# Kernel tuning notes

Hardware: AMD Instinct MI355X
Metric: run time of the kernel (lower is better)

The kernel has to match this reference:

```python
import jax, jax.numpy as jnp
import numpy as np

B, S, E, H = 8, 2048, 1024, 64

def setup_inputs() -> dict:
    key = jax.random.key(0)
    ks = jax.random.split(key, 7)
    scale = 1.0 / np.sqrt(E)
    return {
        "x": jax.random.normal(ks[0], (B, S, E), dtype=jnp.float32),
        "mask": jnp.ones((B, S), dtype=jnp.int32),
        "Wq": jax.random.uniform(ks[1], (E, H), jnp.float32, -scale, scale),
        "bq": jax.random.uniform(ks[2], (H,), jnp.float32, -scale, scale),
        "Wk": jax.random.uniform(ks[3], (E, H), jnp.float32, -scale, scale),
        "bk": jax.random.uniform(ks[4], (H,), jnp.float32, -scale, scale),
        "Wv": jax.random.uniform(ks[5], (E, H), jnp.float32, -scale, scale),
        "bv": jax.random.uniform(ks[6], (H,), jnp.float32, -scale, scale),
    }

def reference(x, mask, Wq, bq, Wk, bk, Wv, bv):
    # q,k,v: [B,S,H]
    q = jnp.einsum('bse,eh->bsh', x, Wq) + bq
    k = jnp.einsum('bse,eh->bsh', x, Wk) + bk
    v = jnp.einsum('bse,eh->bsh', x, Wv) + bv
    # scores: [B,S,S]
    scores = jnp.einsum('bqh,bkh->bqk', q, k) / jnp.sqrt(jnp.asarray(H, q.dtype))
    causal = jnp.tril(jnp.ones((S, S), dtype=bool))  # [S,S]
    pad = (mask != 0)[:, None, :]                    # [B,1,S]
    neg_inf = jnp.asarray(float('-inf'), scores.dtype)
    scores = jnp.where(causal[None] & pad, scores, neg_inf)
    attn = jax.nn.softmax(scores, axis=-1)
    return jnp.einsum('bqk,bkh->bqh', attn, v)
```

## Files before the change

kernel.cpp:

```cpp
#include <hip/hip_runtime.h>
#include <hip/hip_bf16.h>

#define S_ 2048
#define E_ 1024
#define QNC 8

typedef __attribute__((ext_vector_type(8))) short short8;
typedef __attribute__((ext_vector_type(4))) float f32x4;

__device__ __forceinline__ short f2bf(float f) {
    __hip_bfloat16 h = __float2bfloat16(f);
    return *(short*)&h;
}

__device__ __forceinline__ void g2l16(const void* g, void* l) {
    __builtin_amdgcn_global_load_lds(
        (const __attribute__((address_space(1))) void*)g,
        (__attribute__((address_space(3))) void*)l, 16, 0, 0);
}

__global__ __launch_bounds__(256) void prep_weights(
    const float* __restrict__ Wq, const float* __restrict__ Wk,
    const float* __restrict__ Wv, unsigned short* __restrict__ Wtt)
{
    int tw = blockIdx.x * 256 + threadIdx.x;
    int nt = tw >> 11;
    int lane = tw & 63;
    int n = nt * 16 + (lane & 15);
    int h = n & 63;
    const float* W = (n < 64) ? Wq : (n < 128) ? Wk : Wv;
    int k0 = ((tw >> 6) & 31) * 32 + (lane >> 4) * 8;
    short8 o;
    #pragma unroll
    for (int e = 0; e < 8; ++e) o[e] = f2bf(W[(k0 + e) * 64 + h]);
    *(short8*)(Wtt + (size_t)tw * 8) = o;
}

__global__ __launch_bounds__(256) void qkv_main(
    const float* __restrict__ x, const unsigned short* __restrict__ Wtt,
    const float* __restrict__ bq, const float* __restrict__ bk,
    const float* __restrict__ bv,
    unsigned short* __restrict__ Q, unsigned short* __restrict__ K,
    unsigned short* __restrict__ Vt)
{
    __shared__ __align__(16) char lds[3][16384];
    int tid = threadIdx.x;
    int wave = tid >> 6, lane = tid & 63;
    int lo = lane & 15, hi = lane >> 4;
    int wn = wave;
    int rowbase = blockIdx.x * 32;
    const char* xg = (const char*)x;

    f32x4 acc[2][3];
    #pragma unroll
    for (int a = 0; a < 2; ++a)
        #pragma unroll
        for (int j = 0; j < 3; ++j) acc[a][j] = (f32x4){0.f, 0.f, 0.f, 0.f};

    #define STAGE(bb, kc)                                                          \
        {                                                                          \
            _Pragma("unroll")                                                      \
            for (int i = 0; i < 4; ++i) {                                          \
                int u_lin = i * 256 + wave * 64 + lane;                            \
                int r = u_lin >> 5, u = u_lin & 31;                                \
                const char* src = xg + (size_t)(rowbase + r) * 4096 + (kc) * 512   \
                                  + (((u & 24) | ((u & 7) ^ (r & 7))) << 4);       \
                g2l16(src, &lds[bb][(i * 256 + wave * 64) * 16]);                  \
            }                                                                      \
        }

    STAGE(0, 0); STAGE(1, 1); STAGE(2, 2);
    asm volatile("s_waitcnt vmcnt(8)" ::: "memory");
    __builtin_amdgcn_sched_barrier(0);
    __builtin_amdgcn_s_barrier();

    for (int t = 0; t < QNC; ++t) {
        const char* lx = lds[t % 3];

        short8 bfr[3][4];
        #pragma unroll
        for (int j = 0; j < 3; ++j)
            #pragma unroll
            for (int kk = 0; kk < 4; ++kk)
                bfr[j][kk] = *(const short8*)(
                    Wtt + (size_t)(((wn * 3 + j) * 32 + t * 4 + kk) * 64 + lane) * 8);

        #pragma unroll
        for (int rt = 0; rt < 2; ++rt) {
            int r = rt * 16 + lo;
            #pragma unroll
            for (int kk = 0; kk < 4; ++kk) {
                int u0 = kk * 8 + hi * 2;
                float4 a0 = *(const float4*)(lx + r * 512
                               + (((u0 & 24) | ((u0 & 7) ^ (lo & 7))) << 4));
                float4 a1 = *(const float4*)(lx + r * 512
                               + ((((u0 + 1) & 24) | (((u0 + 1) & 7) ^ (lo & 7))) << 4));
                short8 af;
                af[0] = f2bf(a0.x); af[1] = f2bf(a0.y); af[2] = f2bf(a0.z); af[3] = f2bf(a0.w);
                af[4] = f2bf(a1.x); af[5] = f2bf(a1.y); af[6] = f2bf(a1.z); af[7] = f2bf(a1.w);
                #pragma unroll
                for (int j = 0; j < 3; ++j)
                    acc[rt][j] = __builtin_amdgcn_mfma_f32_16x16x32_bf16(af, bfr[j][kk], acc[rt][j], 0, 0, 0);
            }
        }

        __builtin_amdgcn_sched_barrier(0);
        __builtin_amdgcn_s_barrier();
        if (t + 3 < QNC) {
            STAGE(t % 3, t + 3);
            asm volatile("s_waitcnt vmcnt(8)" ::: "memory");
        } else if (t == QNC - 3) {
            asm volatile("s_waitcnt vmcnt(4)" ::: "memory");
        } else if (t == QNC - 2) {
            asm volatile("s_waitcnt vmcnt(0)" ::: "memory");
        }
        __builtin_amdgcn_sched_barrier(0);
        __builtin_amdgcn_s_barrier();
    }
    #undef STAGE

    #pragma unroll
    for (int rt = 0; rt < 2; ++rt) {
        #pragma unroll
        for (int j = 0; j < 3; ++j) {
            int n = wn * 48 + j * 16 + lo;
            #pragma unroll
            for (int r = 0; r < 4; ++r) {
                int row = rowbase + rt * 16 + 4 * hi + r;
                float v = acc[rt][j][r];
                if (n < 64) {
                    Q[(size_t)row * 64 + n] = (unsigned short)f2bf(v + bq[n]);
                } else if (n < 128) {
                    int h = n - 64;
                    K[(size_t)row * 64 + h] = (unsigned short)f2bf(v + bk[h]);
                } else {
                    int h = n - 128;
                    int b = row >> 11, s = row & (S_ - 1);
                    Vt[((size_t)b * 64 + h) * S_ + s] = (unsigned short)f2bf(v + bv[h]);
                }
            }
        }
    }
}

__global__ __launch_bounds__(256) void attn_stage(
    const unsigned short* __restrict__ Q, const unsigned short* __restrict__ K,
    const unsigned short* __restrict__ Vt, const int* __restrict__ mask,
    float* __restrict__ part)
{
    __shared__ __align__(16) char kv[2][16384];
    __shared__ __align__(16) unsigned short p_lds[4][16][72];
    int tid = threadIdx.x;
    int wave = tid >> 6, lane = tid & 63;
    int lo = lane & 15, hi = lane >> 4;
    int blk = blockIdx.x;
    int c = blk & 3;
    int pr = blk >> 2;
    int b = pr & 7;
    int qt64 = 31 - (pr >> 3);
    int nkt = qt64 + 1;
    int chunk = (nkt + 3) >> 2;
    int kt0 = c * chunk;
    int kt1 = min(kt0 + chunk, nkt);
    int ntile = kt1 - kt0;
    int qrow0 = qt64 * 64 + wave * 16;

    f32x4 o[4];
    float ps[4] = {0.f, 0.f, 0.f, 0.f};
    #pragma unroll
    for (int i = 0; i < 4; ++i) o[i] = (f32x4){0.f, 0.f, 0.f, 0.f};

    #define ASTAGE(bb, kt)                                                        \
        {                                                                         \
            int kbase = (kt) * 64;                                                \
            const char* kg = (const char*)K + (size_t)(b * S_ + kbase) * 128;     \
            const char* vg = (const char*)Vt + (size_t)b * 64 * 4096 + kbase * 2; \
            _Pragma("unroll")                                                     \
            for (int j = 0; j < 2; ++j) {                                         \
                int r = (j * 4 + wave) * 8 + (lane >> 3);                         \
                int un = lane & 7;                                                \
                g2l16(kg + r * 128 + ((un ^ (r & 7)) << 4),                       \
                      &kv[bb][(j * 4 + wave) * 1024]);                            \
                g2l16(vg + (size_t)r * 4096 + ((un ^ (r & 7)) << 4),              \
                      &kv[bb][8192 + (j * 4 + wave) * 1024]);                     \
            }                                                                     \
        }

    if (ntile > 0) {
        const unsigned short* qp = Q + ((size_t)(b * S_ + qrow0 + lo)) * 64 + 8 * hi;
        short8 qf0 = *(const short8*)(qp);
        short8 qf1 = *(const short8*)(qp + 32);

        ASTAGE(0, kt0);
        __syncthreads();

        for (int t = 0; t < ntile; ++t) {
            if (t + 1 < ntile) ASTAGE((t + 1) & 1, kt0 + t + 1);

            int kbase = (kt0 + t) * 64;
            const char* kb = kv[t & 1];
            const char* vb = kv[t & 1] + 8192;

            int mv[4];
            #pragma unroll
            for (int nt = 0; nt < 4; ++nt) mv[nt] = mask[b * S_ + kbase + nt * 16 + lo];

            f32x4 s[4];
            #pragma unroll
            for (int i = 0; i < 4; ++i) s[i] = (f32x4){0.f, 0.f, 0.f, 0.f};
            #pragma unroll
            for (int nt = 0; nt < 4; ++nt) {
                short8 kf0 = *(const short8*)(kb + (nt * 16 + lo) * 128 + ((hi ^ (lo & 7)) << 4));
                short8 kf1 = *(const short8*)(kb + (nt * 16 + lo) * 128 + (((4 + hi) ^ (lo & 7)) << 4));
                s[nt] = __builtin_amdgcn_mfma_f32_16x16x32_bf16(qf0, kf0, s[nt], 0, 0, 0);
                s[nt] = __builtin_amdgcn_mfma_f32_16x16x32_bf16(qf1, kf1, s[nt], 0, 0, 0);
            }

            #pragma unroll
            for (int nt = 0; nt < 4; ++nt) {
                int kpos = kbase + nt * 16 + lo;
                #pragma unroll
                for (int r = 0; r < 4; ++r) {
                    int qpos = qrow0 + 4 * hi + r;
                    bool ok = (mv[nt] != 0) && (kpos <= qpos);
                    float pv = ok ? __expf(s[nt][r] * 0.125f) : 0.f;
                    ps[r] += pv;
                    p_lds[wave][4 * hi + r][nt * 16 + lo] = (unsigned short)f2bf(pv);
                }
            }

            #pragma unroll
            for (int kk = 0; kk < 2; ++kk) {
                short8 pf = *(const short8*)&p_lds[wave][lo][kk * 32 + 8 * hi];
                #pragma unroll
                for (int nt = 0; nt < 4; ++nt) {
                    short8 vf = *(const short8*)(vb + (nt * 16 + lo) * 128
                                                 + (((kk * 4 + hi) ^ (lo & 7)) << 4));
                    o[nt] = __builtin_amdgcn_mfma_f32_16x16x32_bf16(pf, vf, o[nt], 0, 0, 0);
                }
            }
            __syncthreads();
        }
    }
    #undef ASTAGE

    float l[4];
    #pragma unroll
    for (int r = 0; r < 4; ++r) {
        float v = ps[r];
        v += __shfl_xor(v, 1);
        v += __shfl_xor(v, 2);
        v += __shfl_xor(v, 4);
        v += __shfl_xor(v, 8);
        l[r] = v;
    }

    int tile16 = b * 128 + qt64 * 4 + wave;
    float* pp = part + (((size_t)c * 1024 + tile16) * 64 + lane) * 20;
    #pragma unroll
    for (int nt = 0; nt < 4; ++nt) *(f32x4*)(pp + nt * 4) = o[nt];
    f32x4 ll;
    #pragma unroll
    for (int r = 0; r < 4; ++r) ll[r] = l[r];
    *(f32x4*)(pp + 16) = ll;
}

__global__ __launch_bounds__(256) void attn_comb(
    const float* __restrict__ part, float* __restrict__ out)
{
    int g = blockIdx.x * 256 + threadIdx.x;
    int tile = g >> 6, lane = g & 63;
    int lo = lane & 15, hi = lane >> 4;
    int b = tile >> 7, qt = tile & 127;
    int qrow0 = qt * 16;

    f32x4 o[4];
    float l[4] = {0.f, 0.f, 0.f, 0.f};
    #pragma unroll
    for (int i = 0; i < 4; ++i) o[i] = (f32x4){0.f, 0.f, 0.f, 0.f};

    #pragma unroll
    for (int c = 0; c < 4; ++c) {
        const float* pp = part + (((size_t)c * 1024 + tile) * 64 + lane) * 20;
        #pragma unroll
        for (int nt = 0; nt < 4; ++nt) {
            f32x4 po = *(const f32x4*)(pp + nt * 4);
            #pragma unroll
            for (int r = 0; r < 4; ++r) o[nt][r] += po[r];
        }
        f32x4 pl = *(const f32x4*)(pp + 16);
        #pragma unroll
        for (int r = 0; r < 4; ++r) l[r] += pl[r];
    }

    #pragma unroll
    for (int nt = 0; nt < 4; ++nt) {
        #pragma unroll
        for (int r = 0; r < 4; ++r) {
            int qpos = qrow0 + 4 * hi + r;
            out[((size_t)(b * S_ + qpos)) * 64 + nt * 16 + lo] =
                (l[r] > 0.f) ? o[nt][r] / l[r] : 0.f;
        }
    }
}

extern "C" void kernel_launch(void* const* d_in, const int* in_sizes, int n_in,
                              void* d_out, int out_size, void* d_ws, size_t ws_size,
                              hipStream_t stream) {
    const float* x   = (const float*)d_in[0];
    const int*   msk = (const int*)d_in[1];
    const float* Wq  = (const float*)d_in[2];
    const float* bq  = (const float*)d_in[3];
    const float* Wk  = (const float*)d_in[4];
    const float* bk  = (const float*)d_in[5];
    const float* Wv  = (const float*)d_in[6];
    const float* bv  = (const float*)d_in[7];
    float* outp = (float*)d_out;

    char* w = (char*)d_ws;
    unsigned short* Wtt = (unsigned short*)w;
    unsigned short* Qb = (unsigned short*)(w + 0x080000);
    unsigned short* Kb = (unsigned short*)(w + 0x280000);
    unsigned short* Vt = (unsigned short*)(w + 0x480000);
    float* partp = (float*)(w + 0x680000);

    prep_weights<<<dim3(96), dim3(256), 0, stream>>>(Wq, Wk, Wv, Wtt);
    qkv_main<<<dim3(512), dim3(256), 0, stream>>>(x, Wtt, bq, bk, bv, Qb, Kb, Vt);
    attn_stage<<<dim3(1024), dim3(256), 0, stream>>>(Qb, Kb, Vt, msk, partp);
    attn_comb<<<dim3(256), dim3(256), 0, stream>>>(partp, outp);
}
```

Baseline: 57.83 us.

## Deepen QKV and attention prefetch pipelines, precompute mask bits

The QKV projection now works on halved K-chunks (16 chunks of 64 floats) through a 5-deep LDS ring. Weight fragments are double-buffered in registers so the next chunk's B loads overlap the current MFMAs, and a launch bound of 4 blocks per CU is requested. The attention kernel moves from double to triple-buffered K/V tiles with explicit vmcnt waits, and it loads all mask values once into a bitmask up front instead of reading the mask each tile. This is meant to hide global-memory latency, at the cost of more LDS in attention, possible register pressure, and hand-tuned waitcnt counts that must match the exact number of loads in flight.

Result: faster. 56.56 us (-2.2%).

```diff
diff --git a/kernel.cpp b/kernel.cpp
--- a/kernel.cpp
+++ b/kernel.cpp
@@ -3,7 +3,7 @@
 
 #define S_ 2048
 #define E_ 1024
-#define QNC 8
+#define QNC 16
 
 typedef __attribute__((ext_vector_type(8))) short short8;
 typedef __attribute__((ext_vector_type(4))) float f32x4;
@@ -36,14 +36,14 @@
     *(short8*)(Wtt + (size_t)tw * 8) = o;
 }
 
-__global__ __launch_bounds__(256) void qkv_main(
+__global__ __launch_bounds__(256, 4) void qkv_main(
     const float* __restrict__ x, const unsigned short* __restrict__ Wtt,
     const float* __restrict__ bq, const float* __restrict__ bk,
     const float* __restrict__ bv,
     unsigned short* __restrict__ Q, unsigned short* __restrict__ K,
     unsigned short* __restrict__ Vt)
 {
-    __shared__ __align__(16) char lds[3][16384];
+    __shared__ __align__(16) char lds[5][8192];
     int tid = threadIdx.x;
     int wave = tid >> 6, lane = tid & 63;
     int lo = lane & 15, hi = lane >> 4;
@@ -57,67 +57,95 @@
         #pragma unroll
         for (int j = 0; j < 3; ++j) acc[a][j] = (f32x4){0.f, 0.f, 0.f, 0.f};
 
-    #define STAGE(bb, kc)                                                          \
-        {                                                                          \
-            _Pragma("unroll")                                                      \
-            for (int i = 0; i < 4; ++i) {                                          \
-                int u_lin = i * 256 + wave * 64 + lane;                            \
-                int r = u_lin >> 5, u = u_lin & 31;                                \
-                const char* src = xg + (size_t)(rowbase + r) * 4096 + (kc) * 512   \
-                                  + (((u & 24) | ((u & 7) ^ (r & 7))) << 4);       \
-                g2l16(src, &lds[bb][(i * 256 + wave * 64) * 16]);                  \
-            }                                                                      \
-        }
-
-    STAGE(0, 0); STAGE(1, 1); STAGE(2, 2);
-    asm volatile("s_waitcnt vmcnt(8)" ::: "memory");
+    #define STAGE(bb, kc)                                                         \
+        {                                                                         \
+            _Pragma("unroll")                                                     \
+            for (int i = 0; i < 2; ++i) {                                         \
+                int u_lin = i * 256 + tid;                                        \
+                int r = u_lin >> 4, u = u_lin & 15;                               \
+                const char* src = xg + (size_t)(rowbase + r) * 4096 + (kc) * 256  \
+                                  + (((u & 8) | ((u & 7) ^ (r & 7))) << 4);       \
+                g2l16(src, &lds[bb][(i * 256 + wave * 64) * 16]);                 \
+            }                                                                     \
+        }
+
+    #define LOADB(dst, t)                                                         \
+        {                                                                         \
+            _Pragma("unroll")                                                     \
+            for (int j = 0; j < 3; ++j)                                           \
+                _Pragma("unroll")                                                 \
+                for (int kk = 0; kk < 2; ++kk)                                    \
+                    dst[j][kk] = *(const short8*)(Wtt +                           \
+                        (size_t)(((wn * 3 + j) * 32 + (t) * 2 + kk) * 64 + lane) * 8); \
+        }
+
+    #define COMPUTE(bfr, t)                                                       \
+        {                                                                         \
+            const char* lx = lds[(t) % 5];                                        \
+            _Pragma("unroll")                                                     \
+            for (int rt = 0; rt < 2; ++rt) {                                      \
+                int r = rt * 16 + lo;                                             \
+                _Pragma("unroll")                                                 \
+                for (int kk = 0; kk < 2; ++kk) {                                  \
+                    int u0 = kk * 8 + hi * 2;                                     \
+                    float4 a0 = *(const float4*)(lx + r * 256                     \
+                        + (((u0 & 8) | ((u0 & 7) ^ (lo & 7))) << 4));             \
+                    float4 a1 = *(const float4*)(lx + r * 256                     \
+                        + ((((u0 + 1) & 8) | (((u0 + 1) & 7) ^ (lo & 7))) << 4)); \
+                    short8 af;                                                    \
+                    af[0] = f2bf(a0.x); af[1] = f2bf(a0.y);                       \
+                    af[2] = f2bf(a0.z); af[3] = f2bf(a0.w);                       \
+                    af[4] = f2bf(a1.x); af[5] = f2bf(a1.y);                       \
+                    af[6] = f2bf(a1.z); af[7] = f2bf(a1.w);                       \
+                    _Pragma("unroll")                                             \
+                    for (int j = 0; j < 3; ++j)                                   \
+                        acc[rt][j] = __builtin_amdgcn_mfma_f32_16x16x32_bf16(     \
+                            af, bfr[j][kk], acc[rt][j], 0, 0, 0);                 \
+                }                                                                 \
+            }                                                                     \
+        }
+
+    #define WAITQ(t)                                                              \
+        {                                                                         \
+            if ((t) <= 11)      asm volatile("s_waitcnt vmcnt(12)" ::: "memory"); \
+            else if ((t) == 12) asm volatile("s_waitcnt vmcnt(10)" ::: "memory"); \
+            else if ((t) == 13) asm volatile("s_waitcnt vmcnt(8)" ::: "memory");  \
+            else                asm volatile("s_waitcnt vmcnt(6)" ::: "memory");  \
+        }
+
+    short8 bfrA[3][2], bfrB[3][2];
+
+    LOADB(bfrA, 0);
+    __builtin_amdgcn_sched_barrier(0);
+    STAGE(0, 0); STAGE(1, 1); STAGE(2, 2); STAGE(3, 3);
+    __builtin_amdgcn_sched_barrier(0);
+    asm volatile("s_waitcnt vmcnt(6)" ::: "memory");
     __builtin_amdgcn_sched_barrier(0);
     __builtin_amdgcn_s_barrier();
 
-    for (int t = 0; t < QNC; ++t) {
-        const char* lx = lds[t % 3];
-
-        short8 bfr[3][4];
-        #pragma unroll
-        for (int j = 0; j < 3; ++j)
-            #pragma unroll
-            for (int kk = 0; kk < 4; ++kk)
-                bfr[j][kk] = *(const short8*)(
-                    Wtt + (size_t)(((wn * 3 + j) * 32 + t * 4 + kk) * 64 + lane) * 8);
-
-        #pragma unroll
-        for (int rt = 0; rt < 2; ++rt) {
-            int r = rt * 16 + lo;
-            #pragma unroll
-            for (int kk = 0; kk < 4; ++kk) {
-                int u0 = kk * 8 + hi * 2;
-                float4 a0 = *(const float4*)(lx + r * 512
-                               + (((u0 & 24) | ((u0 & 7) ^ (lo & 7))) << 4));
-                float4 a1 = *(const float4*)(lx + r * 512
-                               + ((((u0 + 1) & 24) | (((u0 + 1) & 7) ^ (lo & 7))) << 4));
-                short8 af;
-                af[0] = f2bf(a0.x); af[1] = f2bf(a0.y); af[2] = f2bf(a0.z); af[3] = f2bf(a0.w);
-                af[4] = f2bf(a1.x); af[5] = f2bf(a1.y); af[6] = f2bf(a1.z); af[7] = f2bf(a1.w);
-                #pragma unroll
-                for (int j = 0; j < 3; ++j)
-                    acc[rt][j] = __builtin_amdgcn_mfma_f32_16x16x32_bf16(af, bfr[j][kk], acc[rt][j], 0, 0, 0);
-            }
-        }
-
+    for (int tb = 0; tb < 8; ++tb) {
+        int t0 = 2 * tb, t1 = 2 * tb + 1;
+        LOADB(bfrB, t1);
+        COMPUTE(bfrA, t0);
+        if (t0 + 4 < QNC) STAGE((t0 + 4) % 5, t0 + 4);
+        __builtin_amdgcn_sched_barrier(0);
+        WAITQ(t0);
         __builtin_amdgcn_sched_barrier(0);
         __builtin_amdgcn_s_barrier();
-        if (t + 3 < QNC) {
-            STAGE(t % 3, t + 3);
-            asm volatile("s_waitcnt vmcnt(8)" ::: "memory");
-        } else if (t == QNC - 3) {
-            asm volatile("s_waitcnt vmcnt(4)" ::: "memory");
-        } else if (t == QNC - 2) {
-            asm volatile("s_waitcnt vmcnt(0)" ::: "memory");
-        }
-        __builtin_amdgcn_sched_barrier(0);
-        __builtin_amdgcn_s_barrier();
+        if (t1 + 1 < QNC) LOADB(bfrA, t1 + 1);
+        COMPUTE(bfrB, t1);
+        if (t1 + 4 < QNC) STAGE((t1 + 4) % 5, t1 + 4);
+        if (t1 < QNC - 1) {
+            __builtin_amdgcn_sched_barrier(0);
+            WAITQ(t1);
+            __builtin_amdgcn_sched_barrier(0);
+            __builtin_amdgcn_s_barrier();
+        }
     }
     #undef STAGE
+    #undef LOADB
+    #undef COMPUTE
+    #undef WAITQ
 
     #pragma unroll
     for (int rt = 0; rt < 2; ++rt) {
@@ -148,7 +176,7 @@
     const unsigned short* __restrict__ Vt, const int* __restrict__ mask,
     float* __restrict__ part)
 {
-    __shared__ __align__(16) char kv[2][16384];
+    __shared__ __align__(16) char kv[3][16384];
     __shared__ __align__(16) unsigned short p_lds[4][16][72];
     int tid = threadIdx.x;
     int wave = tid >> 6, lane = tid & 63;
@@ -172,9 +200,9 @@
 
     #define ASTAGE(bb, kt)                                                        \
         {                                                                         \
-            int kbase = (kt) * 64;                                                \
-            const char* kg = (const char*)K + (size_t)(b * S_ + kbase) * 128;     \
-            const char* vg = (const char*)Vt + (size_t)b * 64 * 4096 + kbase * 2; \
+            int kbase_ = (kt) * 64;                                               \
+            const char* kg = (const char*)K + (size_t)(b * S_ + kbase_) * 128;    \
+            const char* vg = (const char*)Vt + (size_t)b * 64 * 4096 + kbase_ * 2;\
             _Pragma("unroll")                                                     \
             for (int j = 0; j < 2; ++j) {                                         \
                 int r = (j * 4 + wave) * 8 + (lane >> 3);                         \
@@ -191,19 +219,31 @@
         short8 qf0 = *(const short8*)(qp);
         short8 qf1 = *(const short8*)(qp + 32);
 
+        unsigned mbits = 0;
+        for (int tt = 0; tt < 8; ++tt) {
+            if (tt < ntile) {
+                int kbase = (kt0 + tt) * 64;
+                #pragma unroll
+                for (int nt = 0; nt < 4; ++nt)
+                    if (mask[b * S_ + kbase + nt * 16 + lo] != 0)
+                        mbits |= (1u << (tt * 4 + nt));
+            }
+        }
+        asm volatile("s_waitcnt vmcnt(0)" ::: "memory");
+        __builtin_amdgcn_sched_barrier(0);
+
         ASTAGE(0, kt0);
-        __syncthreads();
+        if (ntile > 1) ASTAGE(1, kt0 + 1);
+        __builtin_amdgcn_sched_barrier(0);
+        if (ntile > 1) asm volatile("s_waitcnt vmcnt(4)" ::: "memory");
+        else           asm volatile("s_waitcnt vmcnt(0)" ::: "memory");
+        __builtin_amdgcn_sched_barrier(0);
+        __builtin_amdgcn_s_barrier();
 
         for (int t = 0; t < ntile; ++t) {
-            if (t + 1 < ntile) ASTAGE((t + 1) & 1, kt0 + t + 1);
-
             int kbase = (kt0 + t) * 64;
-            const char* kb = kv[t & 1];
-            const char* vb = kv[t & 1] + 8192;
-
-            int mv[4];
-            #pragma unroll
-            for (int nt = 0; nt < 4; ++nt) mv[nt] = mask[b * S_ + kbase + nt * 16 + lo];
+            const char* kb = kv[t % 3];
+            const char* vb = kv[t % 3] + 8192;
 
             f32x4 s[4];
             #pragma unroll
@@ -219,10 +259,11 @@
             #pragma unroll
             for (int nt = 0; nt < 4; ++nt) {
                 int kpos = kbase + nt * 16 + lo;
+                bool mok = (mbits >> (t * 4 + nt)) & 1;
                 #pragma unroll
                 for (int r = 0; r < 4; ++r) {
                     int qpos = qrow0 + 4 * hi + r;
-                    bool ok = (mv[nt] != 0) && (kpos <= qpos);
+                    bool ok = mok && (kpos <= qpos);
                     float pv = ok ? __expf(s[nt][r] * 0.125f) : 0.f;
                     ps[r] += pv;
                     p_lds[wave][4 * hi + r][nt * 16 + lo] = (unsigned short)f2bf(pv);
@@ -239,7 +280,15 @@
                     o[nt] = __builtin_amdgcn_mfma_f32_16x16x32_bf16(pf, vf, o[nt], 0, 0, 0);
                 }
             }
-            __syncthreads();
+
+            if (t + 2 < ntile) ASTAGE((t + 2) % 3, kt0 + t + 2);
+            __builtin_amdgcn_sched_barrier(0);
+            if (t + 1 < ntile) {
+                if (t + 2 < ntile) asm volatile("s_waitcnt vmcnt(4)" ::: "memory");
+                else               asm volatile("s_waitcnt vmcnt(0)" ::: "memory");
+                __builtin_amdgcn_sched_barrier(0);
+                __builtin_amdgcn_s_barrier();
+            }
         }
     }
     #undef ASTAGE
```
